# Kernel optimization log

Hardware: AMD Instinct MI355X
Metric: run time of the kernel (lower is better)

The kernel has to match this reference:

```python
import jax, jax.numpy as jnp
import numpy as np

BATCH, IN_DIM, GRID, HID, DEPTH = 2048, 128, 128, 256, 7
BN_EPS = 1e-5


def setup_inputs() -> dict:
    key = jax.random.key(0)
    ks = jax.random.split(key, 10)
    x = jax.random.uniform(ks[0], (BATCH, IN_DIM), dtype=jnp.float32)
    grids = jax.random.uniform(ks[1], (DEPTH, IN_DIM, GRID), dtype=jnp.float32)  # torch.rand init
    fs = jax.random.normal(ks[2], (DEPTH, IN_DIM, GRID, HID), dtype=jnp.float32)
    depth_scores = jnp.ones((DEPTH,), dtype=jnp.float32)
    mlp_W = jax.random.normal(ks[3], (3, HID, HID), dtype=jnp.float32) * (1.0 / np.sqrt(HID))
    mlp_b = jnp.zeros((3, HID), dtype=jnp.float32)
    bn_gamma = jnp.ones((3, HID), dtype=jnp.float32)
    bn_beta = jnp.zeros((3, HID), dtype=jnp.float32)
    W_out = jax.random.normal(ks[4], (HID, 1), dtype=jnp.float32) * (1.0 / np.sqrt(HID))
    b_out = jnp.zeros((1,), dtype=jnp.float32)
    return {"x": x, "grids": grids, "fs": fs, "depth_scores": depth_scores,
            "mlp_W": mlp_W, "mlp_b": mlp_b, "bn_gamma": bn_gamma,
            "bn_beta": bn_beta, "W_out": W_out, "b_out": b_out}


def reference(x, grids, fs, depth_scores, mlp_W, mlp_b, bn_gamma, bn_beta, W_out, b_out):
    # per-feature min-max normalization over the batch dim
    xmin = x.min(axis=0, keepdims=True)
    xmax = x.max(axis=0, keepdims=True)
    z = (x - xmin) / (xmax - xmin + 1e-6)  # [B, I]

    outputs = []
    for i in range(DEPTH):
        Bmat = jax.nn.relu(z[:, :, None] - grids[i][None, :, :])  # [B, I, G]
        # (B.unsqueeze(-1) * fs[i]).sum(2).sum(1) == einsum big,igh->bh
        H = jnp.einsum('big,igh->bh', Bmat, fs[i])  # [B, H]
        if i > 0:  # residual accumulation
            H = H + outputs[-1]
        outputs.append(H)
    stacked = jnp.stack(outputs, axis=0)  # [D, B, H]
    w = jax.nn.softmax(depth_scores)  # depth attention
    h = jnp.einsum('d,dbh->bh', w, stacked)

    # MLP head (BatchNorm uses batch stats = training-mode behaviour; Dropout off)
    for j in range(3):
        h = h @ mlp_W[j] + mlp_b[j]
        mean = h.mean(axis=0)
        var = h.var(axis=0)  # biased, matching torch BN normalization
        h = (h - mean) * jax.lax.rsqrt(var + BN_EPS) * bn_gamma[j] + bn_beta[j]
        h = jax.nn.gelu(h, approximate=False)  # torch nn.GELU is exact erf GELU
    return h @ W_out + b_out
```

## Files before the change

kernel.cpp:

```cpp
#include <hip/hip_runtime.h>
#include <hip/hip_bf16.h>

#define BATCH 2048
#define IN_DIM 128
#define GRIDN 128
#define HID 256
#define DEPTH 7

typedef unsigned int u32;
typedef __attribute__((ext_vector_type(8))) short short8;
typedef __attribute__((ext_vector_type(4))) float floatx4;

#define OFF_FST   ((size_t)0)
#define SZ_FST    ((size_t)7*128*256*128*2)
#define OFF_ZT    (OFF_FST + SZ_FST)
#define SZ_ZT     ((size_t)BATCH*IN_DIM*4)
#define OFF_HPRE  (OFF_ZT + SZ_ZT)
#define SZ_HPRE   ((size_t)BATCH*HID*4)
#define OFF_STATS (OFF_HPRE + SZ_HPRE)
#define SZ_STATS  ((size_t)3*2*HID*4)
#define OFF_KEYS  (OFF_STATS + SZ_STATS)
#define SZ_KEYS   ((size_t)256*4)
#define OFF_CW    (OFF_KEYS + SZ_KEYS)
#define SZ_CW     ((size_t)32)
#define OFF_Y1    (OFF_CW + SZ_CW)
#define SZ_Y      ((size_t)BATCH*HID*4)
#define OFF_Y2    (OFF_Y1 + SZ_Y)
#define OFF_Y3    (OFF_Y2 + SZ_Y)

__device__ __forceinline__ void gload_lds16(const void* g, void* l) {
  __builtin_amdgcn_global_load_lds(
      (const __attribute__((address_space(1))) u32*)g,
      (__attribute__((address_space(3))) u32*)l, 16, 0, 0);
}

__device__ __forceinline__ u32 pack2_bf16(float lo, float hi) {
  __hip_bfloat162 b2;
  b2.x = __float2bfloat16(lo);
  b2.y = __float2bfloat16(hi);
  return *reinterpret_cast<u32*>(&b2);
}

__device__ __forceinline__ u32 pk_trunc(float a, float b) {
  return __builtin_amdgcn_perm(__float_as_uint(b), __float_as_uint(a), 0x07060302u);
}

__device__ __forceinline__ float reluc(float v) {
  return __builtin_amdgcn_fmed3f(v, 0.0f, 1.0f);
}

__device__ __forceinline__ float gelu_exact(float x) {
  return 0.5f * x * (1.0f + erff(x * 0.70710678118654752f));
}

__global__ void prep1_kernel(const float* __restrict__ x, u32* __restrict__ keys,
                             const float* __restrict__ depth_scores,
                             float* __restrict__ cw) {
  int t = threadIdx.x;
  int base = blockIdx.x * 256 + t;
  float mn = 1e30f, mx = -1e30f;
#pragma unroll
  for (int j = 0; j < 16; ++j) {
    float v = x[base + j * 16384];
    mn = fminf(mn, v); mx = fmaxf(mx, v);
  }
  __shared__ float smn[256], smx[256];
  smn[t] = mn; smx[t] = mx;
  __syncthreads();
  if (t < 128) {
    mn = fminf(smn[t], smn[t + 128]);
    mx = fmaxf(smx[t], smx[t + 128]);
    int i = base & 127;
    atomicMax(&keys[i], 0x7FFFFFFFu - __float_as_uint(mn));
    atomicMax(&keys[128 + i], __float_as_uint(mx));
  }
  if (blockIdx.x == 0 && t == 0) {
    float m = -1e30f;
    for (int d0 = 0; d0 < DEPTH; ++d0) m = fmaxf(m, depth_scores[d0]);
    float e[DEPTH]; float sum = 0.f;
    for (int d0 = 0; d0 < DEPTH; ++d0) { e[d0] = expf(depth_scores[d0] - m); sum += e[d0]; }
    float cacc = 0.f; float cs[DEPTH];
    for (int d0 = DEPTH - 1; d0 >= 0; --d0) { cacc += e[d0] / sum; cs[d0] = cacc; }
    for (int d0 = 0; d0 < DEPTH; ++d0) cw[d0] = cs[d0];
  }
}

__global__ void prep2_kernel(const float* __restrict__ x, const u32* __restrict__ keys,
                             float* __restrict__ z_t) {
  __shared__ float lds[128 * 65];
  int t = threadIdx.x;
  int b0 = blockIdx.x * 64;
#pragma unroll
  for (int q = 0; q < 32; ++q) {
    int idx = q * 256 + t;
    int b = idx >> 7, i = idx & 127;
    lds[i * 65 + b] = x[(size_t)(b0 + b) * IN_DIM + i];
  }
  __syncthreads();
#pragma unroll
  for (int q = 0; q < 32; ++q) {
    int idx = q * 256 + t;
    int ii = idx >> 6, bb = idx & 63;
    float mnv = __uint_as_float(0x7FFFFFFFu - keys[ii]);
    float mxv = __uint_as_float(keys[128 + ii]);
    float v = (lds[ii * 65 + bb] - mnv) * (1.0f / (mxv - mnv + 1e-6f));
    z_t[(size_t)ii * BATCH + b0 + bb] = v;
  }
}

__global__ void convert_kernel(const float* __restrict__ fs,
                               const float* __restrict__ cw,
                               __hip_bfloat16* __restrict__ fs2) {
  __shared__ u32 lds[256 * 33];
  int slab = blockIdx.x;
  int t = threadIdx.x;
  float cd = cw[slab >> 7];
  const float* src = fs + (size_t)slab * (GRIDN * HID);
  char* dstb = (char*)fs2 + (size_t)slab * 65536;

  for (int gh = 0; gh < 2; ++gh) {
    const float* s0 = src + (size_t)gh * 64 * HID + t;
#pragma unroll
    for (int g2 = 0; g2 < 32; ++g2) {
      float va = s0[(size_t)(2 * g2) * HID];
      float vb = s0[(size_t)(2 * g2 + 1) * HID];
      lds[t * 33 + g2] = pack2_bf16(cd * va, cd * vb);
    }
    __syncthreads();
#pragma unroll
    for (int it2 = 0; it2 < 8; ++it2) {
      int task = t + it2 * 256;
      int c = task >> 9;
      int q = task & 511;
      int nhalf = c >> 1, ksl = c & 1;
      int tt = q >> 6, l4 = (q >> 4) & 3, l15 = q & 15;
      int h = nhalf * 128 + tt * 16 + l15;
      int m = ksl * 4 + l4;
      u32 a0 = lds[h * 33 + m * 4 + 0];
      u32 a1 = lds[h * 33 + m * 4 + 1];
      u32 a2 = lds[h * 33 + m * 4 + 2];
      u32 a3 = lds[h * 33 + m * 4 + 3];
      size_t off = (size_t)nhalf * 32768 + (size_t)(gh * 2 + ksl) * 8192 +
                   (size_t)tt * 1024 + l4 * 256 + l15 * 16;
      *(uint4*)(dstb + off) = make_uint4(a0, a1, a2, a3);
    }
    __syncthreads();
  }
}

#define FENCE __asm__ volatile("" ::: "memory")
#define WAITV(c) do { __builtin_amdgcn_s_waitcnt(c); FENCE; } while (0)
#define BARR do { FENCE; __builtin_amdgcn_s_barrier(); FENCE; } while (0)
#define VM8 0x0F78
#define VM1 0x0F71
#define VM0 0x0F70

__launch_bounds__(256, 2)
__global__ void gemm_kernel(const float* __restrict__ z_t,
                            const float* __restrict__ grids,
                            const __hip_bfloat16* __restrict__ fs2,
                            float* __restrict__ h_pre) {
  __shared__ __align__(16) char lds[16384];

  int bx = blockIdx.x;
  int xcd = bx & 7;
  int t6 = bx >> 3;
  int cg = t6 >> 4;
  int jb2 = t6 & 15;
  int chunk = xcd + 8 * cg;
  int slab0 = chunk * 28;
  int mt = jb2 >> 1;
  int nh = jb2 & 1;

  int tid = threadIdx.x;
  int w = tid >> 6, l = tid & 63;
  int l15 = l & 15, l4 = l >> 4;
  int mbase = mt * 256 + w * 64;
  int nbase = nh * 128;

  floatx4 acc[4][8];
#pragma unroll
  for (int a = 0; a < 4; ++a)
#pragma unroll
    for (int b = 0; b < 8; ++b) acc[a][b] = (floatx4)0.f;

  const char* fsb = (const char*)fs2 + (size_t)slab0 * 65536 + (size_t)nh * 32768 +
                    (size_t)w * 1024 + (size_t)l * 16;

  auto stage1 = [&](int u) {
    const char* srcb = fsb + (size_t)(u >> 3) * 65536 + (size_t)((u >> 1) & 3) * 8192 +
                       (size_t)(u & 1) * 4096;
    gload_lds16(srcb, lds + (u & 3) * 4096 + w * 1024);
  };

  float4 zA, zB;
  float4 g0A, g1A, g0B, g1B;
  auto zgload = [&](int s, float4& zv, float4& G0, float4& G1) {
    int slab = slab0 + (s >> 2);
    int iz = slab & 127;
    const float* zp = z_t + (size_t)iz * BATCH + mbase + l15;
    zv.x = zp[0]; zv.y = zp[16]; zv.z = zp[32]; zv.w = zp[48];
    const float* gp = grids + (size_t)slab * GRIDN + (s & 3) * 32 + l4 * 8;
    G0 = *(const float4*)gp;
    G1 = *(const float4*)(gp + 4);
  };

  short8 af[4];
  short8 bf[4];
  auto rdfrag = [&](const int bufIdx) {
    const char* bp = lds + bufIdx * 4096 + l * 16;
    bf[0] = *(const short8*)(bp);
    bf[1] = *(const short8*)(bp + 1024);
    bf[2] = *(const short8*)(bp + 2048);
    bf[3] = *(const short8*)(bp + 3072);
  };
  auto afgen = [&](const float4 zv, const float4 G0, const float4 G1) {
#pragma unroll
    for (int u = 0; u < 4; ++u) {
      float zu = (u == 0) ? zv.x : (u == 1) ? zv.y : (u == 2) ? zv.z : zv.w;
      union { uint4 q; short8 s8; } pk;
      pk.q.x = pk_trunc(reluc(zu - G0.x), reluc(zu - G0.y));
      pk.q.y = pk_trunc(reluc(zu - G0.z), reluc(zu - G0.w));
      pk.q.z = pk_trunc(reluc(zu - G1.x), reluc(zu - G1.y));
      pk.q.w = pk_trunc(reluc(zu - G1.z), reluc(zu - G1.w));
      af[u] = pk.s8;
    }
  };
  auto mfma16 = [&](const int ttBase) {
    __builtin_amdgcn_s_setprio(1);
#pragma unroll
    for (int u = 0; u < 4; ++u) {
      acc[u][ttBase + 0] = __builtin_amdgcn_mfma_f32_16x16x32_bf16(af[u], bf[0], acc[u][ttBase + 0], 0, 0, 0);
      acc[u][ttBase + 1] = __builtin_amdgcn_mfma_f32_16x16x32_bf16(af[u], bf[1], acc[u][ttBase + 1], 0, 0, 0);
      acc[u][ttBase + 2] = __builtin_amdgcn_mfma_f32_16x16x32_bf16(af[u], bf[2], acc[u][ttBase + 2], 0, 0, 0);
      acc[u][ttBase + 3] = __builtin_amdgcn_mfma_f32_16x16x32_bf16(af[u], bf[3], acc[u][ttBase + 3], 0, 0, 0);
    }
    __builtin_amdgcn_s_setprio(0);
  };

  zgload(0, zA, g0A, g1A); FENCE;
  stage1(0); stage1(1); stage1(2); FENCE;
  zgload(1, zB, g0B, g1B); FENCE;

#pragma unroll 1
  for (int s = 0; s < 110; s += 2) {
    WAITV(VM8); BARR;
    stage1(2 * s + 3); FENCE;
    afgen(zA, g0A, g1A);
    rdfrag(0);
    mfma16(0);
    WAITV(VM8); BARR;
    stage1(2 * s + 4); FENCE;
    zgload(s + 2, zA, g0A, g1A); FENCE;
    rdfrag(1);
    mfma16(4);
    WAITV(VM8); BARR;
    stage1(2 * s + 5); FENCE;
    afgen(zB, g0B, g1B);
    rdfrag(2);
    mfma16(0);
    WAITV(VM8); BARR;
    stage1(2 * s + 6); FENCE;
    zgload(s + 3, zB, g0B, g1B); FENCE;
    rdfrag(3);
    mfma16(4);
  }

  WAITV(VM8); BARR;
  stage1(223); FENCE;
  afgen(zA, g0A, g1A);
  rdfrag(0);
  mfma16(0);
  WAITV(VM8); BARR;
  rdfrag(1);
  mfma16(4);
  WAITV(VM1); BARR;
  afgen(zB, g0B, g1B);
  rdfrag(2);
  mfma16(0);
  WAITV(VM0); BARR;
  rdfrag(3);
  mfma16(4);

  int row0 = mbase + l4 * 4;
  int col0 = nbase + l15;
#pragma unroll
  for (int u = 0; u < 4; ++u) {
#pragma unroll
    for (int tt = 0; tt < 8; ++tt) {
      int col = col0 + tt * 16;
#pragma unroll
      for (int r = 0; r < 4; ++r) {
        int row = row0 + u * 16 + r;
        atomicAdd(&h_pre[(size_t)row * HID + col], acc[u][tt][r]);
      }
    }
  }
}

template <int FIRST>
__global__ void mlp_kernel(const float* __restrict__ Xin,
                           const float* __restrict__ statsIn,
                           const float* __restrict__ gamma,
                           const float* __restrict__ beta,
                           const float* __restrict__ W,
                           const float* __restrict__ bias,
                           float* __restrict__ Yout,
                           float* __restrict__ statsOut) {
  __shared__ float Xs[4][HID];
  int br = blockIdx.x, c = threadIdx.x;
  float mean = 0.f, rstd = 1.f, gm = 1.f, bt = 0.f;
  if (!FIRST) {
    float s1 = statsIn[c], s2 = statsIn[HID + c];
    mean = s1 * (1.0f / BATCH);
    float var = s2 * (1.0f / BATCH) - mean * mean;
    rstd = rsqrtf(var + 1e-5f);
    gm = gamma[c]; bt = beta[c];
  }
#pragma unroll
  for (int r = 0; r < 4; ++r) {
    float v = Xin[(size_t)(br * 4 + r) * HID + c];
    if (!FIRST) v = gelu_exact((v - mean) * rstd * gm + bt);
    Xs[r][c] = v;
  }
  __syncthreads();
  float acc[4] = {0, 0, 0, 0};
#pragma unroll 8
  for (int k = 0; k < HID; ++k) {
    float wv = W[(size_t)k * HID + c];
#pragma unroll
    for (int r = 0; r < 4; ++r) acc[r] += Xs[r][k] * wv;
  }
  float bb = bias[c];
  float s1 = 0.f, s2 = 0.f;
#pragma unroll
  for (int r = 0; r < 4; ++r) {
    float y = acc[r] + bb;
    Yout[(size_t)(br * 4 + r) * HID + c] = y;
    s1 += y; s2 += y * y;
  }
  atomicAdd(&statsOut[c], s1);
  atomicAdd(&statsOut[HID + c], s2);
}

__global__ void final_kernel(const float* __restrict__ Y3,
                             const float* __restrict__ statsIn,
                             const float* __restrict__ gamma,
                             const float* __restrict__ beta,
                             const float* __restrict__ W_out,
                             const float* __restrict__ b_out,
                             float* __restrict__ out) {
  int w = threadIdx.x >> 6, l = threadIdx.x & 63;
  int b = blockIdx.x * 4 + w;
  float4 y = *(const float4*)(Y3 + (size_t)b * HID + l * 4);
  float4 wv = *(const float4*)(W_out + l * 4);
  float r4[4] = {y.x, y.y, y.z, y.w};
  float w4[4] = {wv.x, wv.y, wv.z, wv.w};
  float s = 0.f;
  int c0 = l * 4;
#pragma unroll
  for (int q = 0; q < 4; ++q) {
    int c = c0 + q;
    float s1 = statsIn[c], s2 = statsIn[HID + c];
    float mean = s1 * (1.0f / BATCH);
    float var = s2 * (1.0f / BATCH) - mean * mean;
    float rstd = rsqrtf(var + 1e-5f);
    float v = gelu_exact((r4[q] - mean) * rstd * gamma[c] + beta[c]);
    s += v * w4[q];
  }
#pragma unroll
  for (int off = 32; off > 0; off >>= 1) s += __shfl_down(s, off);
  if (l == 0) out[b] = s + b_out[0];
}

extern "C" void kernel_launch(void* const* d_in, const int* in_sizes, int n_in,
                              void* d_out, int out_size, void* d_ws, size_t ws_size,
                              hipStream_t stream) {
  const float* x      = (const float*)d_in[0];
  const float* grids  = (const float*)d_in[1];
  const float* fs     = (const float*)d_in[2];
  const float* dscore = (const float*)d_in[3];
  const float* mlp_W  = (const float*)d_in[4];
  const float* mlp_b  = (const float*)d_in[5];
  const float* bn_g   = (const float*)d_in[6];
  const float* bn_b   = (const float*)d_in[7];
  const float* W_out  = (const float*)d_in[8];
  const float* b_out  = (const float*)d_in[9];
  float* out = (float*)d_out;

  char* ws = (char*)d_ws;
  __hip_bfloat16* fs2 = (__hip_bfloat16*)(ws + OFF_FST);
  float* z_t   = (float*)(ws + OFF_ZT);
  float* h_pre = (float*)(ws + OFF_HPRE);
  float* stats = (float*)(ws + OFF_STATS);
  u32*   keys  = (u32*)(ws + OFF_KEYS);
  float* cw    = (float*)(ws + OFF_CW);
  float* Y1    = (float*)(ws + OFF_Y1);
  float* Y2    = (float*)(ws + OFF_Y2);
  float* Y3    = (float*)(ws + OFF_Y3);

  hipMemsetAsync(h_pre, 0, SZ_HPRE + SZ_STATS + SZ_KEYS, stream);

  prep1_kernel<<<64, 256, 0, stream>>>(x, keys, dscore, cw);
  prep2_kernel<<<32, 256, 0, stream>>>(x, keys, z_t);
  convert_kernel<<<DEPTH * IN_DIM, 256, 0, stream>>>(fs, cw, fs2);
  gemm_kernel<<<512, 256, 0, stream>>>(z_t, grids, fs2, h_pre);

  mlp_kernel<1><<<512, 256, 0, stream>>>(h_pre, nullptr, nullptr, nullptr,
                                         mlp_W, mlp_b, Y1, stats);
  mlp_kernel<0><<<512, 256, 0, stream>>>(Y1, stats, bn_g, bn_b,
                                         mlp_W + 65536, mlp_b + 256, Y2, stats + 512);
  mlp_kernel<0><<<512, 256, 0, stream>>>(Y2, stats + 512, bn_g + 256, bn_b + 256,
                                         mlp_W + 2 * 65536, mlp_b + 2 * 256, Y3, stats + 1024);
  final_kernel<<<512, 256, 0, stream>>>(Y3, stats + 1024, bn_g + 512, bn_b + 512,
                                        W_out, b_out, out);
}
```

Measured before the change: 429.0 us.

## Restructure GEMM pipeline to triple-buffered full-K-step stages with one barrier per step

```diff
diff --git a/kernel.cpp b/kernel.cpp
--- a/kernel.cpp
+++ b/kernel.cpp
@@ -152,7 +152,6 @@
 #define WAITV(c) do { __builtin_amdgcn_s_waitcnt(c); FENCE; } while (0)
 #define BARR do { FENCE; __builtin_amdgcn_s_barrier(); FENCE; } while (0)
 #define VM8 0x0F78
-#define VM1 0x0F71
 #define VM0 0x0F70
 
 __launch_bounds__(256, 2)
@@ -160,7 +159,7 @@
                             const float* __restrict__ grids,
                             const __hip_bfloat16* __restrict__ fs2,
                             float* __restrict__ h_pre) {
-  __shared__ __align__(16) char lds[16384];
+  __shared__ __align__(16) char lds[24576];
 
   int bx = blockIdx.x;
   int xcd = bx & 7;
@@ -185,12 +184,13 @@
     for (int b = 0; b < 8; ++b) acc[a][b] = (floatx4)0.f;
 
   const char* fsb = (const char*)fs2 + (size_t)slab0 * 65536 + (size_t)nh * 32768 +
-                    (size_t)w * 1024 + (size_t)l * 16;
-
-  auto stage1 = [&](int u) {
-    const char* srcb = fsb + (size_t)(u >> 3) * 65536 + (size_t)((u >> 1) & 3) * 8192 +
-                       (size_t)(u & 1) * 4096;
-    gload_lds16(srcb, lds + (u & 3) * 4096 + w * 1024);
+                    (size_t)w * 2048 + (size_t)l * 16;
+
+  auto stage8 = [&](int u, int bufIdx) {
+    const char* srcb = fsb + (size_t)(u >> 2) * 65536 + (size_t)(u & 3) * 8192;
+    char* dst = lds + bufIdx * 8192 + w * 2048;
+    gload_lds16(srcb, dst);
+    gload_lds16(srcb + 1024, dst + 1024);
   };
 
   float4 zA, zB;
@@ -206,13 +206,12 @@
   };
 
   short8 af[4];
-  short8 bf[4];
-  auto rdfrag = [&](const int bufIdx) {
-    const char* bp = lds + bufIdx * 4096 + l * 16;
-    bf[0] = *(const short8*)(bp);
-    bf[1] = *(const short8*)(bp + 1024);
-    bf[2] = *(const short8*)(bp + 2048);
-    bf[3] = *(const short8*)(bp + 3072);
+  short8 bf[8];
+  auto rdfrag8 = [&](int bufIdx) {
+    const char* bp = lds + bufIdx * 8192 + l * 16;
+#pragma unroll
+    for (int tt = 0; tt < 8; ++tt)
+      bf[tt] = *(const short8*)(bp + tt * 1024);
   };
   auto afgen = [&](const float4 zv, const float4 G0, const float4 G1) {
 #pragma unroll
@@ -226,61 +225,51 @@
       af[u] = pk.s8;
     }
   };
-  auto mfma16 = [&](const int ttBase) {
+  auto mfma32 = [&]() {
     __builtin_amdgcn_s_setprio(1);
 #pragma unroll
-    for (int u = 0; u < 4; ++u) {
-      acc[u][ttBase + 0] = __builtin_amdgcn_mfma_f32_16x16x32_bf16(af[u], bf[0], acc[u][ttBase + 0], 0, 0, 0);
-      acc[u][ttBase + 1] = __builtin_amdgcn_mfma_f32_16x16x32_bf16(af[u], bf[1], acc[u][ttBase + 1], 0, 0, 0);
-      acc[u][ttBase + 2] = __builtin_amdgcn_mfma_f32_16x16x32_bf16(af[u], bf[2], acc[u][ttBase + 2], 0, 0, 0);
-      acc[u][ttBase + 3] = __builtin_amdgcn_mfma_f32_16x16x32_bf16(af[u], bf[3], acc[u][ttBase + 3], 0, 0, 0);
-    }
+    for (int u = 0; u < 4; ++u)
+#pragma unroll
+      for (int tt = 0; tt < 8; ++tt)
+        acc[u][tt] = __builtin_amdgcn_mfma_f32_16x16x32_bf16(af[u], bf[tt], acc[u][tt], 0, 0, 0);
     __builtin_amdgcn_s_setprio(0);
   };
 
+#define STEP_FULL(S, BUF, STBUF, ZV, G0, G1)                                   \
+  do {                                                                         \
+    WAITV(VM8); BARR;                                                          \
+    stage8((S) + 2, (STBUF)); FENCE;                                           \
+    rdfrag8(BUF);                                                              \
+    afgen(ZV, G0, G1);                                                         \
+    zgload((S) + 2, ZV, G0, G1); FENCE;                                        \
+    mfma32();                                                                  \
+  } while (0)
+
+  stage8(0, 0); FENCE;
   zgload(0, zA, g0A, g1A); FENCE;
-  stage1(0); stage1(1); stage1(2); FENCE;
+  stage8(1, 1); FENCE;
   zgload(1, zB, g0B, g1B); FENCE;
 
 #pragma unroll 1
-  for (int s = 0; s < 110; s += 2) {
-    WAITV(VM8); BARR;
-    stage1(2 * s + 3); FENCE;
-    afgen(zA, g0A, g1A);
-    rdfrag(0);
-    mfma16(0);
-    WAITV(VM8); BARR;
-    stage1(2 * s + 4); FENCE;
-    zgload(s + 2, zA, g0A, g1A); FENCE;
-    rdfrag(1);
-    mfma16(4);
-    WAITV(VM8); BARR;
-    stage1(2 * s + 5); FENCE;
-    afgen(zB, g0B, g1B);
-    rdfrag(2);
-    mfma16(0);
-    WAITV(VM8); BARR;
-    stage1(2 * s + 6); FENCE;
-    zgload(s + 3, zB, g0B, g1B); FENCE;
-    rdfrag(3);
-    mfma16(4);
-  }
-
+  for (int s0 = 0; s0 < 108; s0 += 6) {
+    STEP_FULL(s0 + 0, 0, 2, zA, g0A, g1A);
+    STEP_FULL(s0 + 1, 1, 0, zB, g0B, g1B);
+    STEP_FULL(s0 + 2, 2, 1, zA, g0A, g1A);
+    STEP_FULL(s0 + 3, 0, 2, zB, g0B, g1B);
+    STEP_FULL(s0 + 4, 1, 0, zA, g0A, g1A);
+    STEP_FULL(s0 + 5, 2, 1, zB, g0B, g1B);
+  }
+
+  STEP_FULL(108, 0, 2, zA, g0A, g1A);
+  STEP_FULL(109, 1, 0, zB, g0B, g1B);
   WAITV(VM8); BARR;
-  stage1(223); FENCE;
+  rdfrag8(2);
   afgen(zA, g0A, g1A);
-  rdfrag(0);
-  mfma16(0);
-  WAITV(VM8); BARR;
-  rdfrag(1);
-  mfma16(4);
-  WAITV(VM1); BARR;
+  mfma32();
+  WAITV(VM0); BARR;
+  rdfrag8(0);
   afgen(zB, g0B, g1B);
-  rdfrag(2);
-  mfma16(0);
-  WAITV(VM0); BARR;
-  rdfrag(3);
-  mfma16(4);
+  mfma32();
 
   int row0 = mbase + l4 * 4;
   int col0 = nbase + l15;
```

Measured after the change: 427.5 us. About the same (-0.3%).
